# Kernel tuning notes

Hardware: AMD Instinct MI355X
Metric: run time of the kernel (lower is better)

The kernel has to match this reference:

```python
import jax, jax.numpy as jnp
import numpy as np

N = 50000
E = 800000
F_IN = 96
HID = 96
NCLS = 40


def setup_inputs() -> dict:
    key = jax.random.key(0)
    ks = jax.random.split(key, 10)
    x = jax.random.normal(ks[0], (N, F_IN), dtype=jnp.float32)
    edge_index = jax.random.randint(ks[1], (2, E), 0, N, dtype=jnp.int64)
    def lin(k, fan_in, fan_out):
        kw, kb = jax.random.split(k)
        bound = 1.0 / np.sqrt(fan_in)
        W = jax.random.uniform(kw, (fan_in, fan_out), minval=-bound, maxval=bound, dtype=jnp.float32)
        b = jax.random.uniform(kb, (fan_out,), minval=-bound, maxval=bound, dtype=jnp.float32)
        return W, b
    W1a, b1a = lin(ks[2], F_IN, HID)
    W1b, b1b = lin(ks[3], HID, HID)
    W2a, b2a = lin(ks[4], HID, HID)
    W2b, b2b = lin(ks[5], HID, NCLS)
    return {"x": x, "edge_index": edge_index,
            "W1a": W1a, "b1a": b1a, "W1b": W1b, "b1b": b1b,
            "W2a": W2a, "b2a": b2a, "W2b": W2b, "b2b": b2b}


def _gin_conv(h, src, dst, Wa, ba, Wb, bb):
    # GINConv with eps=0: nn(x + sum_{j->i} x_j); scatter-add over edges.
    agg = jax.ops.segment_sum(h[src], dst, num_segments=N)  # [N, d]
    z = h + agg
    z = jax.nn.relu(z @ Wa + ba)
    return z @ Wb + bb


def reference(x, edge_index, W1a, b1a, W1b, b1b, W2a, b2a, W2b, b2b):
    src, dst = edge_index[0], edge_index[1]
    h = _gin_conv(x, src, dst, W1a, b1a, W1b, b1b)
    h = jax.nn.relu(h)
    out = _gin_conv(h, src, dst, W2a, b2a, W2b, b2b)  # [N, num_classes]
    return out
```

## Files before the change

### kernel.cpp

```cpp
#include <hip/hip_runtime.h>
#include <hip/hip_bf16.h>

#define NODES 50000
#define EDGES 800000
#define FDIM  96
#define NCLS  40

#define NCHK 200
#define CHKE 4000
#define NB   196
#define NCELL (NB * NCHK)
#define SCAN_BLOCKS ((NCELL + 255) / 256)

#define WT_ELEMS (4 * 96 * 96)
#define WT_BLOCKS ((WT_ELEMS + 255) / 256)
#define F2B_N4 (NODES * FDIM / 4)
#define F2B_BLOCKS ((F2B_N4 + 255) / 256)

typedef __attribute__((ext_vector_type(8))) short s8v;
typedef __attribute__((ext_vector_type(4))) float f32x4;

__device__ __forceinline__ float b2f(ushort u) {
  unsigned int x = ((unsigned int)u) << 16;
  union { unsigned int i; float f; } c; c.i = x; return c.f;
}
__device__ __forceinline__ ushort f2b(float f) {
  __hip_bfloat16 b = __float2bfloat16(f);
  return *reinterpret_cast<ushort*>(&b);
}


__global__ __launch_bounds__(256) void count_prep_kernel(const int* __restrict__ dst,
    int* __restrict__ cellCnt,
    const float* __restrict__ W1a, const float* __restrict__ W1b,
    const float* __restrict__ W2a, const float* __restrict__ W2b,
    const float* __restrict__ x,
    ushort* __restrict__ wt, ushort* __restrict__ xb) {
  int t = threadIdx.x;
  if (blockIdx.x < NCHK) {
    __shared__ int hist[NB];
    for (int i = t; i < NB; i += 256) hist[i] = 0;
    __syncthreads();
    int s = blockIdx.x * CHKE;
    for (int i = t; i < CHKE; i += 256) atomicAdd(&hist[dst[s + i] >> 8], 1);
    __syncthreads();
    for (int i = t; i < NB; i += 256) cellCnt[i * NCHK + blockIdx.x] = hist[i];
  } else if (blockIdx.x < NCHK + WT_BLOCKS) {
    int id = (blockIdx.x - NCHK) * 256 + t;
    if (id >= WT_ELEMS) return;
    int m = id / (96 * 96);
    int r = (id % (96 * 96)) / 96;
    int k = id % 96;
    float v = 0.0f;
    if (m == 0) v = W1a[k * 96 + r];
    else if (m == 1) v = W1b[k * 96 + r];
    else if (m == 2) v = W2a[k * 96 + r];
    else if (r < NCLS) v = W2b[k * NCLS + r];
    wt[id] = f2b(v);
  } else {
    int i = (blockIdx.x - NCHK - WT_BLOCKS) * 256 + t;
    if (i < F2B_N4) {
      float4 v = ((const float4*)x)[i];
      ushort4 u;
      u.x = f2b(v.x); u.y = f2b(v.y); u.z = f2b(v.z); u.w = f2b(v.w);
      ((ushort4*)xb)[i] = u;
    }
  }
}


__global__ __launch_bounds__(256) void partial_kernel(const int* __restrict__ a, int n,
                                                      int* __restrict__ partials) {
  __shared__ int sh[256];
  int t = threadIdx.x;
  int idx = blockIdx.x * 256 + t;
  int v = (idx < n) ? a[idx] : 0;
  sh[t] = v;
  __syncthreads();
#pragma unroll
  for (int d = 1; d < 256; d <<= 1) {
    int u = (t >= d) ? sh[t - d] : 0;
    __syncthreads();
    sh[t] += u;
    __syncthreads();
  }
  if (t == 255) partials[blockIdx.x] = sh[255];
}

__global__ __launch_bounds__(256) void scan_partials_kernel(const int* __restrict__ partials,
                                                            int nb, int* __restrict__ poffs) {
  __shared__ int sh[256];
  int t = threadIdx.x;
  int v = (t < nb) ? partials[t] : 0;
  sh[t] = v;
  __syncthreads();
#pragma unroll
  for (int d = 1; d < 256; d <<= 1) {
    int u = (t >= d) ? sh[t - d] : 0;
    __syncthreads();
    sh[t] += u;
    __syncthreads();
  }
  if (t < nb) poffs[t] = sh[t] - v;
}

__global__ __launch_bounds__(256) void final_scan_kernel(const int* __restrict__ a, int n,
                                                         const int* __restrict__ poffs,
                                                         int* __restrict__ out) {
  __shared__ int sh[256];
  int t = threadIdx.x;
  int idx = blockIdx.x * 256 + t;
  int v = (idx < n) ? a[idx] : 0;
  sh[t] = v;
  __syncthreads();
#pragma unroll
  for (int d = 1; d < 256; d <<= 1) {
    int u = (t >= d) ? sh[t - d] : 0;
    __syncthreads();
    sh[t] += u;
    __syncthreads();
  }
  if (idx < n) out[idx] = poffs[blockIdx.x] + sh[t] - v;
}

__global__ __launch_bounds__(256) void bin_scatter_kernel(const int* __restrict__ src,
                                                          const int* __restrict__ dst,
                                                          const int* __restrict__ cellOff,
                                                          int* __restrict__ ebuf) {
  __shared__ int cur[NB];
  int t = threadIdx.x;
  for (int i = t; i < NB; i += 256) cur[i] = cellOff[i * NCHK + blockIdx.x];
  __syncthreads();
  int s = blockIdx.x * CHKE;
  for (int i = t; i < CHKE; i += 256) {
    int d = dst[s + i];
    int pos = atomicAdd(&cur[d >> 8], 1);
    ebuf[pos] = ((d & 255) << 16) | src[s + i];
  }
}

__global__ __launch_bounds__(256) void bucket_sort_kernel(const int* __restrict__ ebuf,
                                                          const int* __restrict__ cellOff,
                                                          int* __restrict__ row_ptr,
                                                          ushort* __restrict__ col) {
  __shared__ int hist[256];
  __shared__ int sh[256];
  int b = blockIdx.x;
  int t = threadIdx.x;
  int s = cellOff[b * NCHK];
  int e = (b + 1 < NB) ? cellOff[(b + 1) * NCHK] : EDGES;
  hist[t] = 0;
  __syncthreads();
  for (int i = s + t; i < e; i += 256) atomicAdd(&hist[ebuf[i] >> 16], 1);
  __syncthreads();
  int v = hist[t];
  sh[t] = v;
  __syncthreads();
#pragma unroll
  for (int d = 1; d < 256; d <<= 1) {
    int u = (t >= d) ? sh[t - d] : 0;
    __syncthreads();
    sh[t] += u;
    __syncthreads();
  }
  int excl = sh[t] - v;
  int node = (b << 8) + t;
  if (node < NODES) row_ptr[node] = s + excl;
  if (node == NODES - 1) row_ptr[NODES] = EDGES;
  hist[t] = excl;
  __syncthreads();
  for (int i = s + t; i < e; i += 256) {
    int ed = ebuf[i];
    int r = atomicAdd(&hist[ed >> 16], 1);
    col[s + r] = (ushort)(ed & 0xFFFF);
  }
}


__global__ __launch_bounds__(256) void aggregate_kernel(const ushort* __restrict__ hin,
    const int* __restrict__ row_ptr, const ushort* __restrict__ col, ushort* __restrict__ z) {
  int gt = blockIdx.x * blockDim.x + threadIdx.x;
  int node = gt >> 6;
  if (node >= NODES) return;
  int lane = threadIdx.x & 63;
  int l = lane & 31;
  int h = lane >> 5;

  float a0 = 0.f, a1 = 0.f, a2 = 0.f;
  if (h == 0) {
    const ushort* self = hin + (size_t)node * FDIM;
    a0 = b2f(self[l]); a1 = b2f(self[l + 32]); a2 = b2f(self[l + 64]);
  }

  int e0 = row_ptr[node];
  int e1 = row_ptr[node + 1];
  int hl = (e1 - e0 + 1) >> 1;
  int e = e0 + h * hl;
  int t = h ? e1 : (e0 + hl);

  for (; e < t; e += 8) {
    const ushort* p8[8];
    float m[8];
#pragma unroll
    for (int q = 0; q < 8; ++q) {
      int idx = e + q;
      bool ok = idx < t;
      int c = col[ok ? idx : t - 1];
      p8[q] = hin + (size_t)c * FDIM;
      m[q] = ok ? 1.0f : 0.0f;
    }
    float s0 = 0.f, s1 = 0.f, s2 = 0.f;
#pragma unroll
    for (int q = 0; q < 8; ++q) {
      s0 = fmaf(m[q], b2f(p8[q][l]), s0);
      s1 = fmaf(m[q], b2f(p8[q][l + 32]), s1);
      s2 = fmaf(m[q], b2f(p8[q][l + 64]), s2);
    }
    a0 += s0; a1 += s1; a2 += s2;
  }

  a0 += __shfl_xor(a0, 32);
  a1 += __shfl_xor(a1, 32);
  a2 += __shfl_xor(a2, 32);

  if (h == 0) {
    ushort* zp = z + (size_t)node * FDIM;
    zp[l] = f2b(a0); zp[l + 32] = f2b(a1); zp[l + 64] = f2b(a2);
  }
}


template <int NOUT2, bool RELU2, bool OUT_BF16>
__global__ __launch_bounds__(256) void gin_mlp_kernel(const ushort* __restrict__ A,
    const ushort* __restrict__ wtA, const float* __restrict__ biasA,
    const ushort* __restrict__ wtB, const float* __restrict__ biasB, void* __restrict__ outv) {
  constexpr int NT2 = (NOUT2 == 96) ? 6 : 3;
  __shared__ ushort sT[64 * 128];

  int lane = threadIdx.x & 63;
  int wave = threadIdx.x >> 6;
  int wrow0 = wave * 16;
  int node0 = blockIdx.x * 64;
  int r = lane & 15;
  int kq = lane >> 4;

  int arow = node0 + wrow0 + r;
  if (arow >= NODES) arow = NODES - 1;
  const ushort* ap = A + (size_t)arow * 96 + kq * 8;
  s8v a0 = *(const s8v*)(ap);
  s8v a1 = *(const s8v*)(ap + 32);
  s8v a2 = *(const s8v*)(ap + 64);

#pragma unroll
  for (int nt = 0; nt < 6; ++nt) {
    int colg = nt * 16 + r;
    const ushort* bp = wtA + (size_t)colg * 96 + kq * 8;
    s8v b0 = *(const s8v*)(bp);
    s8v b1 = *(const s8v*)(bp + 32);
    s8v b2 = *(const s8v*)(bp + 64);
    float bv = biasA[colg];
    f32x4 acc = {bv, bv, bv, bv};
    acc = __builtin_amdgcn_mfma_f32_16x16x32_bf16(a0, b0, acc, 0, 0, 0);
    acc = __builtin_amdgcn_mfma_f32_16x16x32_bf16(a1, b1, acc, 0, 0, 0);
    acc = __builtin_amdgcn_mfma_f32_16x16x32_bf16(a2, b2, acc, 0, 0, 0);
#pragma unroll
    for (int j = 0; j < 4; ++j) {
      int trow = wrow0 + kq * 4 + j;
      float v = fmaxf(acc[j], 0.0f);
      sT[(trow * 128) + (colg ^ ((trow & 7) << 3))] = f2b(v);
    }
  }
  __syncthreads();

  int trow = wrow0 + r;
  int sbase = trow * 128;
  int swz = (trow & 7) << 3;
  s8v c0 = *(const s8v*)&sT[sbase + ((kq * 8 + 0)  ^ swz)];
  s8v c1 = *(const s8v*)&sT[sbase + ((kq * 8 + 32) ^ swz)];
  s8v c2 = *(const s8v*)&sT[sbase + ((kq * 8 + 64) ^ swz)];

#pragma unroll
  for (int nt = 0; nt < NT2; ++nt) {
    int colg = nt * 16 + r;
    const ushort* bp = wtB + (size_t)colg * 96 + kq * 8;
    s8v b0 = *(const s8v*)(bp);
    s8v b1 = *(const s8v*)(bp + 32);
    s8v b2 = *(const s8v*)(bp + 64);
    float bv = (colg < NOUT2) ? biasB[colg] : 0.0f;
    f32x4 acc = {bv, bv, bv, bv};
    acc = __builtin_amdgcn_mfma_f32_16x16x32_bf16(c0, b0, acc, 0, 0, 0);
    acc = __builtin_amdgcn_mfma_f32_16x16x32_bf16(c1, b1, acc, 0, 0, 0);
    acc = __builtin_amdgcn_mfma_f32_16x16x32_bf16(c2, b2, acc, 0, 0, 0);
#pragma unroll
    for (int j = 0; j < 4; ++j) {
      int grow = node0 + wrow0 + kq * 4 + j;
      if (grow < NODES && colg < NOUT2) {
        float v = acc[j];
        if (RELU2) v = fmaxf(v, 0.0f);
        if (OUT_BF16)
          ((ushort*)outv)[(size_t)grow * NOUT2 + colg] = f2b(v);
        else
          ((float*)outv)[(size_t)grow * NOUT2 + colg] = v;
      }
    }
  }
}


extern "C" void kernel_launch(void* const* d_in, const int* in_sizes, int n_in,
                              void* d_out, int out_size, void* d_ws, size_t ws_size,
                              hipStream_t stream) {
  const float* x    = (const float*)d_in[0];
  const int*   ei   = (const int*)d_in[1];
  const float* W1a  = (const float*)d_in[2];
  const float* b1a  = (const float*)d_in[3];
  const float* W1b  = (const float*)d_in[4];
  const float* b1b  = (const float*)d_in[5];
  const float* W2a  = (const float*)d_in[6];
  const float* b2a  = (const float*)d_in[7];
  const float* W2b  = (const float*)d_in[8];
  const float* b2b  = (const float*)d_in[9];
  float* out = (float*)d_out;

  const int* src = ei;
  const int* dst = ei + EDGES;

  char* ws = (char*)d_ws;
  size_t off = 0;
  auto alloc = [&](size_t bytes) {
    size_t p = off;
    off = (off + bytes + 255) & ~(size_t)255;
    return p;
  };
  int*  cellCnt  = (int*)(ws + alloc((size_t)NCELL * 4));
  int*  cellOff  = (int*)(ws + alloc((size_t)NCELL * 4));
  int*  partials = (int*)(ws + alloc((size_t)SCAN_BLOCKS * 4));
  int*  poffs    = (int*)(ws + alloc((size_t)SCAN_BLOCKS * 4));
  int*  row_ptr  = (int*)(ws + alloc((size_t)(NODES + 1) * 4));
  int*  ebuf     = (int*)(ws + alloc((size_t)EDGES * 4));
  ushort* col    = (ushort*)(ws + alloc((size_t)EDGES * 2));
  ushort* wt     = (ushort*)(ws + alloc((size_t)4 * 96 * 96 * 2));
  ushort* xb     = (ushort*)(ws + alloc((size_t)NODES * FDIM * 2));
  ushort* B1     = (ushort*)(ws + alloc((size_t)NODES * FDIM * 2));
  ushort* B2     = (ushort*)(ws + alloc((size_t)NODES * FDIM * 2));

  const int AGG_GRID  = (NODES * 64 + 255) / 256;
  const int GEMM_GRID = (NODES + 63) / 64;

  count_prep_kernel<<<NCHK + WT_BLOCKS + F2B_BLOCKS, 256, 0, stream>>>(
      dst, cellCnt, W1a, W1b, W2a, W2b, x, wt, xb);

  partial_kernel<<<SCAN_BLOCKS, 256, 0, stream>>>(cellCnt, NCELL, partials);
  scan_partials_kernel<<<1, 256, 0, stream>>>(partials, SCAN_BLOCKS, poffs);
  final_scan_kernel<<<SCAN_BLOCKS, 256, 0, stream>>>(cellCnt, NCELL, poffs, cellOff);
  bin_scatter_kernel<<<NCHK, 256, 0, stream>>>(src, dst, cellOff, ebuf);
  bucket_sort_kernel<<<NB, 256, 0, stream>>>(ebuf, cellOff, row_ptr, col);

  aggregate_kernel<<<AGG_GRID, 256, 0, stream>>>(xb, row_ptr, col, B1);
  gin_mlp_kernel<96, true, true><<<GEMM_GRID, 256, 0, stream>>>(
      B1, wt + 0 * 9216, b1a, wt + 1 * 9216, b1b, B2);

  aggregate_kernel<<<AGG_GRID, 256, 0, stream>>>(B2, row_ptr, col, B1);
  gin_mlp_kernel<40, false, false><<<GEMM_GRID, 256, 0, stream>>>(
      B1, wt + 2 * 9216, b2a, wt + 3 * 9216, b2b, out);
}
```

Baseline: 119.4 us.

## Replace three-kernel cell scan with single-block chunk-major scan

Changes the cell count layout to chunk-major and replaces the three-pass global exclusive scan with one single-block kernel. Each thread serially scans its bucket across all 200 chunks, then a block scan of bucket totals supplies the base offset, which is added back in a second pass. This drops two kernel launches and the intermediate partial buffers. In exchange the scan runs on one block, with serial per-thread loops of 200 dependent global reads and writes each, done twice.

```diff
diff --git a/kernel.cpp b/kernel.cpp
--- a/kernel.cpp
+++ b/kernel.cpp
@@ -10,7 +10,6 @@
 #define CHKE 4000
 #define NB   196
 #define NCELL (NB * NCHK)
-#define SCAN_BLOCKS ((NCELL + 255) / 256)
 
 #define WT_ELEMS (4 * 96 * 96)
 #define WT_BLOCKS ((WT_ELEMS + 255) / 256)
@@ -44,7 +43,7 @@
     int s = blockIdx.x * CHKE;
     for (int i = t; i < CHKE; i += 256) atomicAdd(&hist[dst[s + i] >> 8], 1);
     __syncthreads();
-    for (int i = t; i < NB; i += 256) cellCnt[i * NCHK + blockIdx.x] = hist[i];
+    for (int i = t; i < NB; i += 256) cellCnt[blockIdx.x * NB + i] = hist[i];
   } else if (blockIdx.x < NCHK + WT_BLOCKS) {
     int id = (blockIdx.x - NCHK) * 256 + t;
     if (id >= WT_ELEMS) return;
@@ -69,13 +68,19 @@
 }
 
 
-__global__ __launch_bounds__(256) void partial_kernel(const int* __restrict__ a, int n,
-                                                      int* __restrict__ partials) {
+__global__ __launch_bounds__(256) void cell_scan_kernel(const int* __restrict__ cellCnt,
+                                                        int* __restrict__ cellOff) {
   __shared__ int sh[256];
   int t = threadIdx.x;
-  int idx = blockIdx.x * 256 + t;
-  int v = (idx < n) ? a[idx] : 0;
-  sh[t] = v;
+  int tot = 0;
+  if (t < NB) {
+    for (int c = 0; c < NCHK; ++c) {
+      int v = cellCnt[c * NB + t];
+      cellOff[c * NB + t] = tot;
+      tot += v;
+    }
+  }
+  sh[t] = (t < NB) ? tot : 0;
   __syncthreads();
 #pragma unroll
   for (int d = 1; d < 256; d <<= 1) {
@@ -84,43 +89,10 @@
     sh[t] += u;
     __syncthreads();
   }
-  if (t == 255) partials[blockIdx.x] = sh[255];
-}
-
-__global__ __launch_bounds__(256) void scan_partials_kernel(const int* __restrict__ partials,
-                                                            int nb, int* __restrict__ poffs) {
-  __shared__ int sh[256];
-  int t = threadIdx.x;
-  int v = (t < nb) ? partials[t] : 0;
-  sh[t] = v;
-  __syncthreads();
-#pragma unroll
-  for (int d = 1; d < 256; d <<= 1) {
-    int u = (t >= d) ? sh[t - d] : 0;
-    __syncthreads();
-    sh[t] += u;
-    __syncthreads();
-  }
-  if (t < nb) poffs[t] = sh[t] - v;
-}
-
-__global__ __launch_bounds__(256) void final_scan_kernel(const int* __restrict__ a, int n,
-                                                         const int* __restrict__ poffs,
-                                                         int* __restrict__ out) {
-  __shared__ int sh[256];
-  int t = threadIdx.x;
-  int idx = blockIdx.x * 256 + t;
-  int v = (idx < n) ? a[idx] : 0;
-  sh[t] = v;
-  __syncthreads();
-#pragma unroll
-  for (int d = 1; d < 256; d <<= 1) {
-    int u = (t >= d) ? sh[t - d] : 0;
-    __syncthreads();
-    sh[t] += u;
-    __syncthreads();
-  }
-  if (idx < n) out[idx] = poffs[blockIdx.x] + sh[t] - v;
+  int base = sh[t] - tot;
+  if (t < NB) {
+    for (int c = 0; c < NCHK; ++c) cellOff[c * NB + t] += base;
+  }
 }
 
 __global__ __launch_bounds__(256) void bin_scatter_kernel(const int* __restrict__ src,
@@ -129,7 +101,7 @@
                                                           int* __restrict__ ebuf) {
   __shared__ int cur[NB];
   int t = threadIdx.x;
-  for (int i = t; i < NB; i += 256) cur[i] = cellOff[i * NCHK + blockIdx.x];
+  for (int i = t; i < NB; i += 256) cur[i] = cellOff[blockIdx.x * NB + i];
   __syncthreads();
   int s = blockIdx.x * CHKE;
   for (int i = t; i < CHKE; i += 256) {
@@ -147,8 +119,8 @@
   __shared__ int sh[256];
   int b = blockIdx.x;
   int t = threadIdx.x;
-  int s = cellOff[b * NCHK];
-  int e = (b + 1 < NB) ? cellOff[(b + 1) * NCHK] : EDGES;
+  int s = cellOff[b];
+  int e = (b + 1 < NB) ? cellOff[b + 1] : EDGES;
   hist[t] = 0;
   __syncthreads();
   for (int i = s + t; i < e; i += 256) atomicAdd(&hist[ebuf[i] >> 16], 1);
@@ -334,8 +306,6 @@
   };
   int*  cellCnt  = (int*)(ws + alloc((size_t)NCELL * 4));
   int*  cellOff  = (int*)(ws + alloc((size_t)NCELL * 4));
-  int*  partials = (int*)(ws + alloc((size_t)SCAN_BLOCKS * 4));
-  int*  poffs    = (int*)(ws + alloc((size_t)SCAN_BLOCKS * 4));
   int*  row_ptr  = (int*)(ws + alloc((size_t)(NODES + 1) * 4));
   int*  ebuf     = (int*)(ws + alloc((size_t)EDGES * 4));
   ushort* col    = (ushort*)(ws + alloc((size_t)EDGES * 2));
@@ -350,9 +320,7 @@
   count_prep_kernel<<<NCHK + WT_BLOCKS + F2B_BLOCKS, 256, 0, stream>>>(
       dst, cellCnt, W1a, W1b, W2a, W2b, x, wt, xb);
 
-  partial_kernel<<<SCAN_BLOCKS, 256, 0, stream>>>(cellCnt, NCELL, partials);
-  scan_partials_kernel<<<1, 256, 0, stream>>>(partials, SCAN_BLOCKS, poffs);
-  final_scan_kernel<<<SCAN_BLOCKS, 256, 0, stream>>>(cellCnt, NCELL, poffs, cellOff);
+  cell_scan_kernel<<<1, 256, 0, stream>>>(cellCnt, cellOff);
   bin_scatter_kernel<<<NCHK, 256, 0, stream>>>(src, dst, cellOff, ebuf);
   bucket_sort_kernel<<<NB, 256, 0, stream>>>(ebuf, cellOff, row_ptr, col);
 
```

Result: slower. 150.6 us (+26.1%).
